# Kernel tuning notes

Measured on AMD Instinct MI355X. Metric: run time of the kernel, lower is better.

Reference implementation:

```python
import jax, jax.numpy as jnp
import numpy as np

B, S, D, H, FF = 2, 2048, 1024, 16, 4096
DH = D // H  # head dim


def _layernorm(x, g, b, eps=1e-5):
    m = x.mean(-1, keepdims=True)
    v = ((x - m) ** 2).mean(-1, keepdims=True)
    return (x - m) / jnp.sqrt(v + eps) * g + b


def setup_inputs() -> dict:
    key = jax.random.key(0)
    ks = jax.random.split(key, 10)
    s = 0.02
    return {
        "x": jax.random.normal(ks[0], (B, S, D), jnp.float32),
        "y": jax.random.normal(ks[1], (B, S, D), jnp.float32),
        "z": jax.random.normal(ks[2], (B, S, D), jnp.float32),
        "mask": jnp.ones((B, 1, S, S), jnp.int32),
        "Wq": jax.random.normal(ks[3], (D, D), jnp.float32) * s,
        "bq": jnp.zeros((D,), jnp.float32),
        "Wk": jax.random.normal(ks[4], (D, D), jnp.float32) * s,
        "bk": jnp.zeros((D,), jnp.float32),
        "Wv": jax.random.normal(ks[5], (D, D), jnp.float32) * s,
        "bv": jnp.zeros((D,), jnp.float32),
        "Wo": jax.random.normal(ks[6], (D, D), jnp.float32) * s,
        "bo": jnp.zeros((D,), jnp.float32),
        "W1": jax.random.normal(ks[7], (D, FF), jnp.float32) * s,
        "b1": jnp.zeros((FF,), jnp.float32),
        "W2": jax.random.normal(ks[8], (FF, D), jnp.float32) * s,
        "b2": jnp.zeros((D,), jnp.float32),
        "ln_g": jnp.ones((D,), jnp.float32),
        "ln_b": jnp.zeros((D,), jnp.float32),
    }


def reference(x, y, z, mask, Wq, bq, Wk, bk, Wv, bv, Wo, bo, W1, b1, W2, b2, ln_g, ln_b):
    q = (x @ Wq + bq).reshape(B, S, H, DH)
    k = (y @ Wk + bk).reshape(B, S, H, DH)
    v = (z @ Wv + bv).reshape(B, S, H, DH)
    # scores: [B, H, Q, K]
    scores = jnp.einsum('bqhl,bkhl->bhqk', q, k) / (DH ** 0.5)
    scores = jnp.where(mask == 0, jnp.float32(-1e10), scores)
    # NOTE: source softmaxes over dim=2 (the query axis) -- faithful.
    p = jax.nn.softmax(scores, axis=2)
    # Source einsum 'bhqk,bvhl->bvhl' sums p over q,k -> per-(b,h) scalar scaling v.
    s_bh = p.sum(axis=(2, 3))  # [B, H]
    att = s_bh[:, None, :, None] * v  # [B, S, H, DH]
    att = att.reshape(B, S, D) @ Wo + bo
    # shared AddAndNorm (same LayerNorm params used twice); dropout = identity (eval)
    h1 = _layernorm(z + att, ln_g, ln_b)
    ff = jax.nn.relu(h1 @ W1 + b1) @ W2 + b2
    return _layernorm(h1 + ff, ln_g, ln_b)
```

## Files before the change

### kernel.cpp

```cpp
#include <hip/hip_runtime.h>

static constexpr int kB = 2, kS = 2048, kD = 1024, kFF = 4096;
static constexpr int kM = kB * kS;
static constexpr size_t MB = 1u << 20;

typedef __attribute__((ext_vector_type(8))) short short8;
typedef __attribute__((ext_vector_type(4))) float f32x4;

__device__ __forceinline__ unsigned short f2bf(float f) {
  union { float f; unsigned int u; } c; c.f = f;
  unsigned int u = c.u;
  unsigned int r = u + 0x7FFFu + ((u >> 16) & 1u);
  return (unsigned short)(r >> 16);
}

__device__ __forceinline__ float bf2f(unsigned short b) {
  union { unsigned int u; float f; } c;
  c.u = ((unsigned int)b) << 16;
  return c.f;
}

__device__ __forceinline__ void gload_lds16(const void* g, void* l) {
  __builtin_amdgcn_global_load_lds(
      (const __attribute__((address_space(1))) void*)g,
      (__attribute__((address_space(3))) void*)l, 16, 0, 0);
}

__global__ __launch_bounds__(256) void cast_bf16_kernel(
    const float* __restrict__ in, unsigned short* __restrict__ out, int n) {
  int i = (blockIdx.x * 256 + threadIdx.x) * 4;
  if (i >= n) return;
  float4 v = *(const float4*)(in + i);
  ushort4 o;
  o.x = f2bf(v.x); o.y = f2bf(v.y); o.z = f2bf(v.z); o.w = f2bf(v.w);
  *(ushort4*)(out + i) = o;
}

__global__ __launch_bounds__(256) void cast_transpose64(
    const float* __restrict__ W, unsigned short* __restrict__ Wt,
    int K, int N, float scale, int ntN) {
  __shared__ float tile[64][65];
  const int bid = blockIdx.x;
  const int nb = (bid % ntN) * 64, kb = (bid / ntN) * 64;
  const int tx = threadIdx.x & 15, ty = threadIdx.x >> 4;
#pragma unroll
  for (int p = 0; p < 4; ++p) {
    const int r = ty + 16 * p;
    float4 v = *(const float4*)(W + (size_t)(kb + r) * N + nb + tx * 4);
    tile[r][tx * 4 + 0] = v.x;
    tile[r][tx * 4 + 1] = v.y;
    tile[r][tx * 4 + 2] = v.z;
    tile[r][tx * 4 + 3] = v.w;
  }
  __syncthreads();
#pragma unroll
  for (int p = 0; p < 4; ++p) {
    const int n = ty + 16 * p;
    ushort4 o;
    o.x = f2bf(tile[tx * 4 + 0][n] * scale);
    o.y = f2bf(tile[tx * 4 + 1][n] * scale);
    o.z = f2bf(tile[tx * 4 + 2][n] * scale);
    o.w = f2bf(tile[tx * 4 + 3][n] * scale);
    *(ushort4*)(Wt + (size_t)(nb + n) * K + kb + tx * 4) = o;
  }
}

__global__ __launch_bounds__(256) void bias_gemv_part_kernel(
    const float* __restrict__ bv, const float* __restrict__ Wo,
    float* __restrict__ partial) {
  const int b = blockIdx.x, t = threadIdx.x;
  const int c = t * 4;
  float4 acc = {0.f, 0.f, 0.f, 0.f};
#pragma unroll
  for (int r = 0; r < 8; ++r) {
    const int f = b * 8 + r;
    const float s = bv[f];
    float4 w = *(const float4*)(Wo + (size_t)f * 1024 + c);
    acc.x = fmaf(s, w.x, acc.x);
    acc.y = fmaf(s, w.y, acc.y);
    acc.z = fmaf(s, w.z, acc.z);
    acc.w = fmaf(s, w.w, acc.w);
  }
  *(float4*)(partial + (size_t)b * 1024 + c) = acc;
}

__global__ __launch_bounds__(256) void bias_gemv_fin_kernel(
    const float* __restrict__ partial, const float* __restrict__ bo,
    float* __restrict__ bc) {
  const int n = blockIdx.x * 256 + threadIdx.x;
  float acc = 0.0f;
#pragma unroll 8
  for (int b = 0; b < 128; ++b) acc += partial[(size_t)b * 1024 + n];
  bc[n] = 2048.0f * acc + bo[n];
}

template <int OUT_BF16, int RELU, int ADD_I, int A_F32>
__global__ __launch_bounds__(256, 4) void gemm_bt(
    const void* __restrict__ A, const unsigned short* __restrict__ Bt,
    const float* __restrict__ bias, void* __restrict__ Cout,
    int M, int N, int K, int nXtiles, int nTilesPerSplit, int kSplitLen,
    size_t cStride, int cr, int cc) {
  __shared__ __align__(16) unsigned short sA[128 * 64];
  __shared__ __align__(16) unsigned short sB[128 * 64];
  const unsigned short* Ab = (const unsigned short*)A;
  const float* Af = (const float*)A;
  const int tid = threadIdx.x;
  const int wave = tid >> 6, lane = tid & 63;
  const int wr = wave >> 1, wc = wave & 1;

  const int x = blockIdx.x & 7, j = blockIdx.x >> 3;
  const int bpc = cr * cc;
  const int chunkIdx = x + 8 * (j / bpc);
  const int w = j % bpc;
  const int chunksPerSplit = nTilesPerSplit / bpc;
  const int split = chunkIdx / chunksPerSplit;
  const int cL = chunkIdx % chunksPerSplit;
  const int cpr = nXtiles / cc;
  const int m0 = ((cL / cpr) * cr + w / cc) * 128;
  const int n0 = ((cL % cpr) * cc + w % cc) * 128;
  const int kBeg = split * kSplitLen, kEnd = kBeg + kSplitLen;

  const int srow = lane >> 3;
  const int scol = ((lane & 7) ^ srow) * 8;

  f32x4 acc[4][4] = {};

  for (int k0 = kBeg; k0 < kEnd; k0 += 64) {
    if constexpr (A_F32) {
      float4 pa[4][2];
#pragma unroll
      for (int i = 0; i < 4; ++i) {
        const int chunk = i * 4 + wave;
        const int rr = chunk * 8 + srow;
        const float* az = Af + (size_t)(m0 + rr) * K + (k0 + scol);
        pa[i][0] = *(const float4*)az;
        pa[i][1] = *(const float4*)(az + 4);
      }
#pragma unroll
      for (int i = 0; i < 4; ++i) {
        const int chunk = i * 4 + wave;
        short8 cv;
        cv[0] = (short)f2bf(pa[i][0].x); cv[1] = (short)f2bf(pa[i][0].y);
        cv[2] = (short)f2bf(pa[i][0].z); cv[3] = (short)f2bf(pa[i][0].w);
        cv[4] = (short)f2bf(pa[i][1].x); cv[5] = (short)f2bf(pa[i][1].y);
        cv[6] = (short)f2bf(pa[i][1].z); cv[7] = (short)f2bf(pa[i][1].w);
        *(short8*)&sA[chunk * 512 + lane * 8] = cv;
      }
    } else {
#pragma unroll
      for (int i = 0; i < 4; ++i) {
        const int chunk = i * 4 + wave;
        const int rr = chunk * 8 + srow;
        gload_lds16(Ab + (size_t)(m0 + rr) * K + (k0 + scol), &sA[chunk * 512]);
      }
    }
#pragma unroll
    for (int i = 0; i < 4; ++i) {
      const int chunk = i * 4 + wave;
      const int rr = chunk * 8 + srow;
      gload_lds16(Bt + (size_t)(n0 + rr) * K + (k0 + scol), &sB[chunk * 512]);
    }
    __syncthreads();
#pragma unroll
    for (int kk = 0; kk < 64; kk += 32) {
      const int kcol = kk + (lane >> 4) * 8;
      const int kswz = (lane & 7) * 8;
      short8 af[4], bfr[4];
#pragma unroll
      for (int m = 0; m < 4; ++m)
        af[m] = *(const short8*)&sA[(wr * 64 + m * 16 + (lane & 15)) * 64 + (kcol ^ kswz)];
#pragma unroll
      for (int n = 0; n < 4; ++n)
        bfr[n] = *(const short8*)&sB[(wc * 64 + n * 16 + (lane & 15)) * 64 + (kcol ^ kswz)];
#pragma unroll
      for (int m = 0; m < 4; ++m)
#pragma unroll
        for (int n = 0; n < 4; ++n)
          acc[m][n] = __builtin_amdgcn_mfma_f32_16x16x32_bf16(af[m], bfr[n], acc[m][n], 0, 0, 0);
    }
    __syncthreads();
  }

  const int cl = lane & 15, rg = lane >> 4;
  const float* bptr = (split == 0) ? bias : nullptr;
#pragma unroll
  for (int n = 0; n < 4; ++n) {
    const int col = n0 + wc * 64 + n * 16 + cl;
    const float bias_v = bptr ? bptr[col] : 0.0f;
#pragma unroll
    for (int m = 0; m < 4; ++m) {
      const int rbase = m0 + wr * 64 + m * 16 + rg * 4;
#pragma unroll
      for (int j2 = 0; j2 < 4; ++j2) {
        float v = acc[m][n][j2] + bias_v;
        if (ADD_I && (rbase + j2 == col)) v += 1.0f;
        if (RELU) v = fmaxf(v, 0.0f);
        const size_t idx = split * cStride + (size_t)(rbase + j2) * N + col;
        if (OUT_BF16)
          ((unsigned short*)Cout)[idx] = f2bf(v);
        else
          ((float*)Cout)[idx] = v;
      }
    }
  }
}

__global__ __launch_bounds__(256) void ln2_bf16_kernel(
    const unsigned short* __restrict__ P, size_t pStr,
    const float* __restrict__ gg, const float* __restrict__ bb,
    unsigned short* __restrict__ Hb) {
  const int row = blockIdx.x, t = threadIdx.x;
  const size_t base = (size_t)row * 1024 + t * 4;
  ushort4 v0 = *(const ushort4*)(P + base);
  ushort4 v1 = *(const ushort4*)(P + pStr + base);
  float a0 = bf2f(v0.x) + bf2f(v1.x);
  float a1 = bf2f(v0.y) + bf2f(v1.y);
  float a2 = bf2f(v0.z) + bf2f(v1.z);
  float a3 = bf2f(v0.w) + bf2f(v1.w);
  float s = a0 + a1 + a2 + a3;
  float ss = a0 * a0 + a1 * a1 + a2 * a2 + a3 * a3;
#pragma unroll
  for (int off = 32; off > 0; off >>= 1) {
    s += __shfl_down(s, off);
    ss += __shfl_down(ss, off);
  }
  __shared__ float rs[4], rss[4];
  __shared__ float smean, srstd;
  const int wave = t >> 6, lane = t & 63;
  if (lane == 0) { rs[wave] = s; rss[wave] = ss; }
  __syncthreads();
  if (t == 0) {
    float S1 = rs[0] + rs[1] + rs[2] + rs[3];
    float S2 = rss[0] + rss[1] + rss[2] + rss[3];
    float mean = S1 * (1.0f / 1024.0f);
    float var = S2 * (1.0f / 1024.0f) - mean * mean;
    smean = mean;
    srstd = rsqrtf(var + 1e-5f);
  }
  __syncthreads();
  const float mean = smean, rstd = srstd;
  float4 gv = *(const float4*)(gg + t * 4);
  float4 bv = *(const float4*)(bb + t * 4);
  ushort4 hb;
  hb.x = f2bf((a0 - mean) * rstd * gv.x + bv.x);
  hb.y = f2bf((a1 - mean) * rstd * gv.y + bv.y);
  hb.z = f2bf((a2 - mean) * rstd * gv.z + bv.z);
  hb.w = f2bf((a3 - mean) * rstd * gv.w + bv.w);
  *(ushort4*)(Hb + base) = hb;
}

__global__ __launch_bounds__(256) void ln_fin4_kernel(
    const unsigned short* __restrict__ Res, const unsigned short* __restrict__ P,
    size_t pStr, const float* __restrict__ gg, const float* __restrict__ bb,
    float* __restrict__ out) {
  const int row = blockIdx.x, t = threadIdx.x;
  const size_t base = (size_t)row * 1024 + t * 4;
  ushort4 rv = *(const ushort4*)(Res + base);
  ushort4 v0 = *(const ushort4*)(P + base);
  ushort4 v1 = *(const ushort4*)(P + pStr + base);
  ushort4 v2 = *(const ushort4*)(P + 2 * pStr + base);
  ushort4 v3 = *(const ushort4*)(P + 3 * pStr + base);
  float a0 = bf2f(rv.x) + bf2f(v0.x) + bf2f(v1.x) + bf2f(v2.x) + bf2f(v3.x);
  float a1 = bf2f(rv.y) + bf2f(v0.y) + bf2f(v1.y) + bf2f(v2.y) + bf2f(v3.y);
  float a2 = bf2f(rv.z) + bf2f(v0.z) + bf2f(v1.z) + bf2f(v2.z) + bf2f(v3.z);
  float a3 = bf2f(rv.w) + bf2f(v0.w) + bf2f(v1.w) + bf2f(v2.w) + bf2f(v3.w);
  float s = a0 + a1 + a2 + a3;
  float ss = a0 * a0 + a1 * a1 + a2 * a2 + a3 * a3;
#pragma unroll
  for (int off = 32; off > 0; off >>= 1) {
    s += __shfl_down(s, off);
    ss += __shfl_down(ss, off);
  }
  __shared__ float rs[4], rss[4];
  __shared__ float smean, srstd;
  const int wave = t >> 6, lane = t & 63;
  if (lane == 0) { rs[wave] = s; rss[wave] = ss; }
  __syncthreads();
  if (t == 0) {
    float S1 = rs[0] + rs[1] + rs[2] + rs[3];
    float S2 = rss[0] + rss[1] + rss[2] + rss[3];
    float mean = S1 * (1.0f / 1024.0f);
    float var = S2 * (1.0f / 1024.0f) - mean * mean;
    smean = mean;
    srstd = rsqrtf(var + 1e-5f);
  }
  __syncthreads();
  const float mean = smean, rstd = srstd;
  float4 gv = *(const float4*)(gg + t * 4);
  float4 bv = *(const float4*)(bb + t * 4);
  float4 ov;
  ov.x = (a0 - mean) * rstd * gv.x + bv.x;
  ov.y = (a1 - mean) * rstd * gv.y + bv.y;
  ov.z = (a2 - mean) * rstd * gv.z + bv.z;
  ov.w = (a3 - mean) * rstd * gv.w + bv.w;
  *(float4*)(out + base) = ov;
}

extern "C" void kernel_launch(void* const* d_in, const int* in_sizes, int n_in,
                              void* d_out, int out_size, void* d_ws, size_t ws_size,
                              hipStream_t stream) {
  const float* z  = (const float*)d_in[2];
  const float* Wv = (const float*)d_in[8];
  const float* bv = (const float*)d_in[9];
  const float* Wo = (const float*)d_in[10];
  const float* bo = (const float*)d_in[11];
  const float* W1 = (const float*)d_in[12];
  const float* b1 = (const float*)d_in[13];
  const float* W2 = (const float*)d_in[14];
  const float* b2 = (const float*)d_in[15];
  const float* lng = (const float*)d_in[16];
  const float* lnb = (const float*)d_in[17];
  float* out = (float*)d_out;

  char* ws = (char*)d_ws;
  unsigned short* a1   = (unsigned short*)(ws + 0 * MB);
  unsigned short* attP = (unsigned short*)(ws + 32 * MB);
  unsigned short* ffP  = (unsigned short*)(ws + 32 * MB);
  unsigned short* W2T  = (unsigned short*)(ws + 64 * MB);
  unsigned short* WoT  = (unsigned short*)(ws + 88 * MB);
  unsigned short* WvBf = (unsigned short*)(ws + 90 * MB);
  unsigned short* WcT  = (unsigned short*)(ws + 92 * MB);
  float*          bc   = (float*)(ws + 94 * MB);
  float*          bprt = (float*)(ws + 94 * MB + 65536);
  unsigned short* h1bf = (unsigned short*)(ws + 96 * MB);
  unsigned short* W1T  = (unsigned short*)(ws + 104 * MB);

  const size_t pStr = (size_t)kM * kD;

  cast_transpose64<<<dim3(256), dim3(256), 0, stream>>>(
      Wo, WoT, kD, kD, (float)kS, kD / 64);
  cast_bf16_kernel<<<dim3(kD * kD / 1024), dim3(256), 0, stream>>>(Wv, WvBf, kD * kD);
  bias_gemv_part_kernel<<<dim3(128), dim3(256), 0, stream>>>(bv, Wo, bprt);
  bias_gemv_fin_kernel<<<dim3(4), dim3(256), 0, stream>>>(bprt, bo, bc);

  gemm_bt<1, 0, 1, 0><<<dim3(64), dim3(256), 0, stream>>>(
      WoT, WvBf, nullptr, WcT, kD, kD, kD, kD / 128, 64, kD, 0, 4, 2);

  gemm_bt<1, 0, 0, 1><<<dim3(512), dim3(256), 0, stream>>>(
      z, WcT, bc, attP, kM, kD, kD, kD / 128, 256, 512, pStr, 8, 8);

  ln2_bf16_kernel<<<dim3(kM), dim3(256), 0, stream>>>(attP, pStr, lng, lnb, h1bf);

  cast_transpose64<<<dim3(1024), dim3(256), 0, stream>>>(
      W1, W1T, kD, kFF, 1.0f, kFF / 64);
  gemm_bt<1, 1, 0, 0><<<dim3(1024), dim3(256), 0, stream>>>(
      h1bf, W1T, b1, a1, kM, kFF, kD, kFF / 128, 1024, kD, 0, 16, 8);

  cast_transpose64<<<dim3(1024), dim3(256), 0, stream>>>(
      W2, W2T, kFF, kD, 1.0f, kD / 64);
  gemm_bt<1, 0, 0, 0><<<dim3(1024), dim3(256), 0, stream>>>(
      a1, W2T, b2, ffP, kM, kD, kFF, kD / 128, 256, kFF / 4, pStr, 16, 8);

  ln_fin4_kernel<<<dim3(kM), dim3(256), 0, stream>>>(h1bf, ffP, pStr, lng, lnb, out);
}
```

Before: 163.7 us.

## Increase split-K for weight-combine and attention GEMMs, add partial-sum reductions

After: 159.8 us. 2.4% less time.

```diff
diff --git a/kernel.cpp b/kernel.cpp
--- a/kernel.cpp
+++ b/kernel.cpp
@@ -94,7 +94,24 @@
   bc[n] = 2048.0f * acc + bo[n];
 }
 
-template <int OUT_BF16, int RELU, int ADD_I, int A_F32>
+__global__ __launch_bounds__(256) void combine_wc4_kernel(
+    const unsigned short* __restrict__ P, unsigned short* __restrict__ Wt) {
+  const int i = (blockIdx.x * 256 + threadIdx.x) * 4;
+  const int MN = 1024 * 1024;
+  ushort4 s0 = *(const ushort4*)(P + i);
+  ushort4 s1 = *(const ushort4*)(P + MN + i);
+  ushort4 s2 = *(const ushort4*)(P + 2 * MN + i);
+  ushort4 s3 = *(const ushort4*)(P + 3 * MN + i);
+  const int row = i >> 10, col = i & 1023;
+  float v0 = bf2f(s0.x) + bf2f(s1.x) + bf2f(s2.x) + bf2f(s3.x) + (row == col + 0 ? 1.0f : 0.0f);
+  float v1 = bf2f(s0.y) + bf2f(s1.y) + bf2f(s2.y) + bf2f(s3.y) + (row == col + 1 ? 1.0f : 0.0f);
+  float v2 = bf2f(s0.z) + bf2f(s1.z) + bf2f(s2.z) + bf2f(s3.z) + (row == col + 2 ? 1.0f : 0.0f);
+  float v3 = bf2f(s0.w) + bf2f(s1.w) + bf2f(s2.w) + bf2f(s3.w) + (row == col + 3 ? 1.0f : 0.0f);
+  ushort4 o; o.x = f2bf(v0); o.y = f2bf(v1); o.z = f2bf(v2); o.w = f2bf(v3);
+  *(ushort4*)(Wt + i) = o;
+}
+
+template <int OUT_BF16, int RELU, int A_F32>
 __global__ __launch_bounds__(256, 4) void gemm_bt(
     const void* __restrict__ A, const unsigned short* __restrict__ Bt,
     const float* __restrict__ bias, void* __restrict__ Cout,
@@ -193,7 +210,6 @@
 #pragma unroll
       for (int j2 = 0; j2 < 4; ++j2) {
         float v = acc[m][n][j2] + bias_v;
-        if (ADD_I && (rbase + j2 == col)) v += 1.0f;
         if (RELU) v = fmaxf(v, 0.0f);
         const size_t idx = split * cStride + (size_t)(rbase + j2) * N + col;
         if (OUT_BF16)
@@ -205,7 +221,7 @@
   }
 }
 
-__global__ __launch_bounds__(256) void ln2_bf16_kernel(
+__global__ __launch_bounds__(256) void ln4_bf16_kernel(
     const unsigned short* __restrict__ P, size_t pStr,
     const float* __restrict__ gg, const float* __restrict__ bb,
     unsigned short* __restrict__ Hb) {
@@ -213,10 +229,12 @@
   const size_t base = (size_t)row * 1024 + t * 4;
   ushort4 v0 = *(const ushort4*)(P + base);
   ushort4 v1 = *(const ushort4*)(P + pStr + base);
-  float a0 = bf2f(v0.x) + bf2f(v1.x);
-  float a1 = bf2f(v0.y) + bf2f(v1.y);
-  float a2 = bf2f(v0.z) + bf2f(v1.z);
-  float a3 = bf2f(v0.w) + bf2f(v1.w);
+  ushort4 v2 = *(const ushort4*)(P + 2 * pStr + base);
+  ushort4 v3 = *(const ushort4*)(P + 3 * pStr + base);
+  float a0 = bf2f(v0.x) + bf2f(v1.x) + bf2f(v2.x) + bf2f(v3.x);
+  float a1 = bf2f(v0.y) + bf2f(v1.y) + bf2f(v2.y) + bf2f(v3.y);
+  float a2 = bf2f(v0.z) + bf2f(v1.z) + bf2f(v2.z) + bf2f(v3.z);
+  float a3 = bf2f(v0.w) + bf2f(v1.w) + bf2f(v2.w) + bf2f(v3.w);
   float s = a0 + a1 + a2 + a3;
   float ss = a0 * a0 + a1 * a1 + a2 * a2 + a3 * a3;
 #pragma unroll
@@ -316,6 +334,7 @@
   unsigned short* a1   = (unsigned short*)(ws + 0 * MB);
   unsigned short* attP = (unsigned short*)(ws + 32 * MB);
   unsigned short* ffP  = (unsigned short*)(ws + 32 * MB);
+  unsigned short* wcpB = (unsigned short*)(ws + 64 * MB);
   unsigned short* W2T  = (unsigned short*)(ws + 64 * MB);
   unsigned short* WoT  = (unsigned short*)(ws + 88 * MB);
   unsigned short* WvBf = (unsigned short*)(ws + 90 * MB);
@@ -326,6 +345,7 @@
   unsigned short* W1T  = (unsigned short*)(ws + 104 * MB);
 
   const size_t pStr = (size_t)kM * kD;
+  const size_t wStr = (size_t)kD * kD;
 
   cast_transpose64<<<dim3(256), dim3(256), 0, stream>>>(
       Wo, WoT, kD, kD, (float)kS, kD / 64);
@@ -333,22 +353,23 @@
   bias_gemv_part_kernel<<<dim3(128), dim3(256), 0, stream>>>(bv, Wo, bprt);
   bias_gemv_fin_kernel<<<dim3(4), dim3(256), 0, stream>>>(bprt, bo, bc);
 
-  gemm_bt<1, 0, 1, 0><<<dim3(64), dim3(256), 0, stream>>>(
-      WoT, WvBf, nullptr, WcT, kD, kD, kD, kD / 128, 64, kD, 0, 4, 2);
-
-  gemm_bt<1, 0, 0, 1><<<dim3(512), dim3(256), 0, stream>>>(
-      z, WcT, bc, attP, kM, kD, kD, kD / 128, 256, 512, pStr, 8, 8);
-
-  ln2_bf16_kernel<<<dim3(kM), dim3(256), 0, stream>>>(attP, pStr, lng, lnb, h1bf);
+  gemm_bt<1, 0, 0><<<dim3(256), dim3(256), 0, stream>>>(
+      WoT, WvBf, nullptr, wcpB, kD, kD, kD, kD / 128, 64, 256, wStr, 8, 4);
+  combine_wc4_kernel<<<dim3(1024), dim3(256), 0, stream>>>(wcpB, WcT);
+
+  gemm_bt<1, 0, 1><<<dim3(1024), dim3(256), 0, stream>>>(
+      z, WcT, bc, attP, kM, kD, kD, kD / 128, 256, 256, pStr, 8, 8);
+
+  ln4_bf16_kernel<<<dim3(kM), dim3(256), 0, stream>>>(attP, pStr, lng, lnb, h1bf);
 
   cast_transpose64<<<dim3(1024), dim3(256), 0, stream>>>(
       W1, W1T, kD, kFF, 1.0f, kFF / 64);
-  gemm_bt<1, 1, 0, 0><<<dim3(1024), dim3(256), 0, stream>>>(
+  gemm_bt<1, 1, 0><<<dim3(1024), dim3(256), 0, stream>>>(
       h1bf, W1T, b1, a1, kM, kFF, kD, kFF / 128, 1024, kD, 0, 16, 8);
 
   cast_transpose64<<<dim3(1024), dim3(256), 0, stream>>>(
       W2, W2T, kFF, kD, 1.0f, kD / 64);
-  gemm_bt<1, 0, 0, 0><<<dim3(1024), dim3(256), 0, stream>>>(
+  gemm_bt<1, 0, 0><<<dim3(1024), dim3(256), 0, stream>>>(
       a1, W2T, b2, ffP, kM, kD, kFF, kD / 128, 256, kFF / 4, pStr, 16, 8);
 
   ln_fin4_kernel<<<dim3(kM), dim3(256), 0, stream>>>(h1bf, ffP, pStr, lng, lnb, out);
```
